# Optimization experiments

Measured on AMD Instinct MI355X. Metric: run time of the kernel, lower is better.

The kernel has to match this reference:

```python
import jax, jax.numpy as jnp
import numpy as np

N = 50000
E = 600000
IN, HID, OUT = 128, 128, 64
EPS = 1e-5

def setup_inputs() -> dict:
    key = jax.random.key(0)
    ks = jax.random.split(key, 16)
    def lin(k, i, o):
        s = 1.0 / np.sqrt(i)
        return jax.random.uniform(k, (i, o), jnp.float32, -s, s)
    inp = {
        "x": jax.random.normal(ks[0], (N, IN), jnp.float32),
        "edge_index": jax.random.randint(ks[1], (2, E), 0, N, jnp.int32),
        "edge_weight": jax.random.uniform(ks[2], (E,), jnp.float32),
        # SAGEConv params: lin_l (aggregated neighbors, with bias), lin_r (root)
        "Wl0": lin(ks[3], IN, HID), "Wr0": lin(ks[4], IN, HID), "b0": jnp.zeros((HID,), jnp.float32),
        "Wl1": lin(ks[5], HID, HID), "Wr1": lin(ks[6], HID, HID), "b1": jnp.zeros((HID,), jnp.float32),
        "Wl2": lin(ks[7], HID, OUT), "Wr2": lin(ks[8], HID, OUT), "b2": jnp.zeros((OUT,), jnp.float32),
        "gamma0": jnp.ones((HID,), jnp.float32), "beta0": jnp.zeros((HID,), jnp.float32),
        "gamma1": jnp.ones((HID,), jnp.float32), "beta1": jnp.zeros((HID,), jnp.float32),
    }
    return inp

def _sage_conv(x, src, dst, w, Wl, Wr, b):
    # weighted message m_e = w_e * x[src_e], mean-aggregated at dst
    msg = x[src] * w[:, None]                                   # [E, F]
    agg = jax.ops.segment_sum(msg, dst, num_segments=N)          # [N, F]
    cnt = jax.ops.segment_sum(jnp.ones_like(w), dst, num_segments=N)
    mean = agg / jnp.maximum(cnt, 1.0)[:, None]
    return mean @ Wl + b + x @ Wr

def _bn(x, gamma, beta):
    mu = jnp.mean(x, axis=0)
    var = jnp.var(x, axis=0)
    return (x - mu) * jax.lax.rsqrt(var + EPS) * gamma + beta

def reference(x, edge_index, edge_weight,
              Wl0, Wr0, b0, Wl1, Wr1, b1, Wl2, Wr2, b2,
              gamma0, beta0, gamma1, beta1):
    src, dst = edge_index[0], edge_index[1]
    h = _sage_conv(x, src, dst, edge_weight, Wl0, Wr0, b0)
    h = jax.nn.relu(_bn(h, gamma0, beta0))  # dropout: identity in eval
    h = _sage_conv(h, src, dst, edge_weight, Wl1, Wr1, b1)
    h = jax.nn.relu(_bn(h, gamma1, beta1))
    return _sage_conv(h, src, dst, edge_weight, Wl2, Wr2, b2)
```

## Files before the change

### kernel.cpp

```cpp
#include <hip/hip_runtime.h>
#include <hip/hip_bf16.h>

#define NN 50000
#define EE 600000
#define SREP 64
#define SCB 49

typedef short bf16x8 __attribute__((ext_vector_type(8)));
typedef float f32x4 __attribute__((ext_vector_type(4)));

__device__ inline ushort f2bf(float x) {
  unsigned u = __float_as_uint(x);
  u = (u + 0x7fffu + ((u >> 16) & 1u)) >> 16;
  return (ushort)u;
}
__device__ inline float bflo(uint t) { return __uint_as_float(t << 16); }
__device__ inline float bfhi(uint t) { return __uint_as_float(t & 0xffff0000u); }
__device__ inline uint f22bf(float a, float b) { return ((uint)f2bf(b) << 16) | (uint)f2bf(a); }

__global__ void count_k(const int* __restrict__ ei, int* __restrict__ cnt_d) {
  int e = blockIdx.x * 256 + threadIdx.x;
  if (e < EE) atomicAdd(&cnt_d[ei[EE + e]], 1);
}

__global__ __launch_bounds__(256) void scanA_k(const int* __restrict__ cnt,
                                               int* __restrict__ cur,
                                               int* __restrict__ bsum) {
  __shared__ int ls[256];
  const int t = threadIdx.x;
  const int base = blockIdx.x * 1024 + t * 4;
  int4 v = {0, 0, 0, 0};
  if (base + 3 < NN) v = *(const int4*)(cnt + base);
  else {
    if (base + 0 < NN) v.x = cnt[base + 0];
    if (base + 1 < NN) v.y = cnt[base + 1];
    if (base + 2 < NN) v.z = cnt[base + 2];
  }
  ls[t] = v.x + v.y + v.z + v.w;
  __syncthreads();
  for (int off = 1; off < 256; off <<= 1) {
    int u = (t >= off) ? ls[t - off] : 0;
    __syncthreads();
    ls[t] += u;
    __syncthreads();
  }
  int ex = (t == 0) ? 0 : ls[t - 1];
  int4 o;
  o.x = ex;
  o.y = ex + v.x;
  o.z = o.y + v.y;
  o.w = o.z + v.z;
  if (base + 3 < NN) *(int4*)(cur + base) = o;
  else {
    if (base + 0 < NN) cur[base + 0] = o.x;
    if (base + 1 < NN) cur[base + 1] = o.y;
    if (base + 2 < NN) cur[base + 2] = o.z;
  }
  if (t == 255) bsum[blockIdx.x] = ls[255];
}

__global__ __launch_bounds__(64) void scanB_k(int* __restrict__ bsum) {
  int t = threadIdx.x;
  int own = (t < SCB) ? bsum[t] : 0;
  int v = own;
#pragma unroll
  for (int off = 1; off < 64; off <<= 1) {
    int u = __shfl_up(v, off, 64);
    if (t >= off) v += u;
  }
  if (t < SCB) bsum[t] = v - own;
}

__global__ __launch_bounds__(256) void scanC_k(int* __restrict__ cur,
                                               const int* __restrict__ bsum,
                                               const int* __restrict__ cnt_d,
                                               int* __restrict__ rowp,
                                               float* __restrict__ invd) {
  const int t = threadIdx.x;
  const int base = blockIdx.x * 1024 + t * 4;
  const int off = bsum[blockIdx.x];
  if (base + 3 < NN) {
    int4 v = *(int4*)(cur + base);
    v.x += off; v.y += off; v.z += off; v.w += off;
    *(int4*)(cur + base) = v;
    *(int4*)(rowp + base) = v;
    int4 cd = *(const int4*)(cnt_d + base);
    float4 iv;
    iv.x = 1.0f / (float)max(cd.x, 1);
    iv.y = 1.0f / (float)max(cd.y, 1);
    iv.z = 1.0f / (float)max(cd.z, 1);
    iv.w = 1.0f / (float)max(cd.w, 1);
    *(float4*)(invd + base) = iv;
  } else {
    for (int i = 0; i < 4; ++i) {
      if (base + i < NN) {
        int v = cur[base + i] + off;
        cur[base + i] = v;
        rowp[base + i] = v;
        invd[base + i] = 1.0f / (float)max(cnt_d[base + i], 1);
      }
    }
  }
}

__global__ void fill_k(const int* __restrict__ ei, const float* __restrict__ ew,
                       int* __restrict__ cur_d, int2* __restrict__ eL) {
  int e = blockIdx.x * 256 + threadIdx.x;
  if (e < EE) {
    int s = ei[e], d = ei[EE + e];
    int pc = atomicAdd(&cur_d[d], 1);
    int2 v;
    v.x = s;
    v.y = __float_as_int(ew[e]);
    eL[pc] = v;
  }
}

__global__ void wpk_k(const float* __restrict__ Wl0, const float* __restrict__ Wr0,
                      const float* __restrict__ Wl1, const float* __restrict__ Wr1,
                      const float* __restrict__ Wl2, const float* __restrict__ Wr2,
                      ushort* __restrict__ wbuf) {
  int idx = blockIdx.x * 256 + threadIdx.x;
  const float* W; int F, r, off;
  if (idx < 16384)      { W = Wl0; F = 128; r = idx;         off = 0; }
  else if (idx < 32768) { W = Wr0; F = 128; r = idx - 16384; off = 16384; }
  else if (idx < 49152) { W = Wl1; F = 128; r = idx - 32768; off = 32768; }
  else if (idx < 65536) { W = Wr1; F = 128; r = idx - 49152; off = 49152; }
  else if (idx < 73728) { W = Wl2; F = 64;  r = idx - 65536; off = 65536; }
  else                  { W = Wr2; F = 64;  r = idx - 73728; off = 73728; }
  int k = r / F, n = r % F;
  wbuf[off + n * 128 + ((((k >> 3) + n) & 15) << 3) + (k & 7)] = f2bf(W[k * F + n]);
}

template <int F, bool HB16>
__global__ __launch_bounds__(256) void gemm_mfma(
    const void* __restrict__ H, const ushort* __restrict__ Wpre,
    const float* __restrict__ ss, ushort* __restrict__ Tlb,
    ushort* __restrict__ Trb) {
  __shared__ __align__(16) ushort Wt[F * 128];
  const int tid = threadIdx.x;
  const int lane = tid & 63;
  const int w = tid >> 6;
  const int col = lane & 15;
  const int quad = lane >> 4;
  const int nb = blockIdx.x * 128;

  bf16x8 afrag[2][4];
#pragma unroll
  for (int t2 = 0; t2 < 2; ++t2) {
    const int row = nb + w * 32 + t2 * 16 + col;
#pragma unroll
    for (int s = 0; s < 4; ++s) {
      const int c = s * 4 + quad;
      const int gk = c * 8;
      uint4 hv = {0, 0, 0, 0};
      if (HB16) {
        if (row < NN) hv = *(const uint4*)((const ushort*)H + (size_t)row * 128 + gk);
        uint* p = (uint*)&hv;
#pragma unroll
        for (int j = 0; j < 4; ++j) {
          float f0 = fmaxf(fmaf(bflo(p[j]), ss[gk + 2 * j], ss[128 + gk + 2 * j]), 0.f);
          float f1 = fmaxf(fmaf(bfhi(p[j]), ss[gk + 2 * j + 1], ss[128 + gk + 2 * j + 1]), 0.f);
          p[j] = f22bf(f0, f1);
        }
      } else {
        float4 fa = {0.f, 0.f, 0.f, 0.f}, fb = {0.f, 0.f, 0.f, 0.f};
        if (row < NN) {
          fa = *(const float4*)((const float*)H + (size_t)row * 128 + gk);
          fb = *(const float4*)((const float*)H + (size_t)row * 128 + gk + 4);
        }
        uint* p = (uint*)&hv;
        p[0] = f22bf(fa.x, fa.y);
        p[1] = f22bf(fa.z, fa.w);
        p[2] = f22bf(fb.x, fb.y);
        p[3] = f22bf(fb.z, fb.w);
      }
      afrag[t2][s] = *(const bf16x8*)&hv;
    }
  }

  for (int phase = 0; phase < 2; ++phase) {
    const uint4* src = (const uint4*)(Wpre + phase * F * 128);
    __syncthreads();
    for (int i = tid; i < F * 16; i += 256) ((uint4*)Wt)[i] = src[i];
    __syncthreads();
    ushort* Outp = phase ? Trb : Tlb;
#pragma unroll 2
    for (int ct = 0; ct < F / 16; ++ct) {
      const int n = ct * 16 + col;
      f32x4 acc0 = {0.f, 0.f, 0.f, 0.f};
      f32x4 acc1 = {0.f, 0.f, 0.f, 0.f};
#pragma unroll
      for (int s = 0; s < 4; ++s) {
        const int c = s * 4 + quad;
        bf16x8 b = *(const bf16x8*)&Wt[n * 128 + (((c + n) & 15) << 3)];
        acc0 = __builtin_amdgcn_mfma_f32_16x16x32_bf16(afrag[0][s], b, acc0, 0, 0, 0);
        acc1 = __builtin_amdgcn_mfma_f32_16x16x32_bf16(afrag[1][s], b, acc1, 0, 0, 0);
      }
      const int cc = ct * 16 + col;
      const int nodeb0 = nb + w * 32 + quad * 4;
#pragma unroll
      for (int r = 0; r < 4; ++r) {
        const int node = nodeb0 + r;
        if (node < NN) Outp[(size_t)node * F + cc] = f2bf(acc0[r]);
      }
#pragma unroll
      for (int r = 0; r < 4; ++r) {
        const int node = nodeb0 + 16 + r;
        if (node < NN) Outp[(size_t)node * F + cc] = f2bf(acc1[r]);
      }
    }
  }
}

template <int F, bool STATS, bool OUTF32>
__global__ __launch_bounds__(256, 8) void gather_combine(
    const ushort* __restrict__ Tlb, const int2* __restrict__ eL,
    const int* __restrict__ rowp, const int* __restrict__ cnt_d,
    const ushort* __restrict__ Trb, const float* __restrict__ invd,
    const float* __restrict__ bias, void* __restrict__ outp,
    float* __restrict__ statsb) {
  constexpr int L = F / 2;
  constexpr int NPI = 256 / L;
  constexpr int NPB = (L == 64) ? 20 : 16;
  const int tid = threadIdx.x;
  const int cp = tid % L;
  const int c = 2 * cp;
  const int nl = tid / L;
  const int n0 = blockIdx.x * NPB;
  const float bx = bias[c], by = bias[c + 1];
  float2 S = {0.f, 0.f}, Q = {0.f, 0.f};
#pragma unroll
  for (int it = 0; it < NPB / NPI; ++it) {
    int n = n0 + it * NPI + nl;
    if constexpr (L == 64) n = __builtin_amdgcn_readfirstlane(n);
    const int beg = rowp[n];
    const int deg = cnt_d[n];
    float a0 = 0.f, a1 = 0.f;
    for (int base = 0; base < deg; base += L) {
      const int take = deg - base;
      int2 er = {0, 0};
      if (cp < take) er = eL[beg + base + cp];
      int m = take < L ? take : L;
      if constexpr (L == 32) m = max(m, __shfl_xor(m, 32, 64));
      int j = 0;
      for (; j + 4 <= m; j += 4) {
        int s0 = __shfl(er.x, j + 0, L);
        int s1 = __shfl(er.x, j + 1, L);
        int s2 = __shfl(er.x, j + 2, L);
        int s3 = __shfl(er.x, j + 3, L);
        float w0 = __int_as_float(__shfl(er.y, j + 0, L));
        float w1 = __int_as_float(__shfl(er.y, j + 1, L));
        float w2 = __int_as_float(__shfl(er.y, j + 2, L));
        float w3 = __int_as_float(__shfl(er.y, j + 3, L));
        uint t0 = ((const uint*)Tlb)[(size_t)s0 * L + cp];
        uint t1 = ((const uint*)Tlb)[(size_t)s1 * L + cp];
        uint t2 = ((const uint*)Tlb)[(size_t)s2 * L + cp];
        uint t3 = ((const uint*)Tlb)[(size_t)s3 * L + cp];
        a0 = fmaf(w0, bflo(t0), a0); a1 = fmaf(w0, bfhi(t0), a1);
        a0 = fmaf(w1, bflo(t1), a0); a1 = fmaf(w1, bfhi(t1), a1);
        a0 = fmaf(w2, bflo(t2), a0); a1 = fmaf(w2, bfhi(t2), a1);
        a0 = fmaf(w3, bflo(t3), a0); a1 = fmaf(w3, bfhi(t3), a1);
      }
      for (; j < m; ++j) {
        int s0 = __shfl(er.x, j, L);
        float w0 = __int_as_float(__shfl(er.y, j, L));
        uint t0 = ((const uint*)Tlb)[(size_t)s0 * L + cp];
        a0 = fmaf(w0, bflo(t0), a0);
        a1 = fmaf(w0, bfhi(t0), a1);
      }
    }
    float iv = invd[n];
    uint tb = ((const uint*)Trb)[(size_t)n * L + cp];
    float2 v;
    v.x = fmaf(a0, iv, bflo(tb) + bx);
    v.y = fmaf(a1, iv, bfhi(tb) + by);
    if (OUTF32) *(float2*)((float*)outp + (size_t)n * F + c) = v;
    else ((uint*)outp)[(size_t)n * L + cp] = f22bf(v.x, v.y);
    if constexpr (STATS) {
      S.x += v.x; S.y += v.y;
      Q.x += v.x * v.x; Q.y += v.y * v.y;
    }
  }
  if constexpr (STATS) {
    __shared__ float2 sS[4][L];
    __shared__ float2 sQ[4][L];
    const int wid = tid >> 6, wl = tid & 63;
    if constexpr (L == 64) {
      sS[wid][wl] = S;
      sQ[wid][wl] = Q;
    } else {
      S.x += __shfl_xor(S.x, 32, 64); S.y += __shfl_xor(S.y, 32, 64);
      Q.x += __shfl_xor(Q.x, 32, 64); Q.y += __shfl_xor(Q.y, 32, 64);
      if (wl < 32) { sS[wid][wl] = S; sQ[wid][wl] = Q; }
    }
    __syncthreads();
    if (tid < L) {
      float2 Sa = sS[0][tid], Qa = sQ[0][tid];
#pragma unroll
      for (int w2 = 1; w2 < 4; ++w2) {
        Sa.x += sS[w2][tid].x; Sa.y += sS[w2][tid].y;
        Qa.x += sQ[w2][tid].x; Qa.y += sQ[w2][tid].y;
      }
      float* sb = statsb + (size_t)(blockIdx.x & (SREP - 1)) * 256;
      int col = 2 * tid;
      atomicAdd(&sb[col], Sa.x);
      atomicAdd(&sb[col + 1], Sa.y);
      atomicAdd(&sb[128 + col], Qa.x);
      atomicAdd(&sb[128 + col + 1], Qa.y);
    }
  }
}

__global__ void bn_fin(float* __restrict__ statsb, const float* __restrict__ gamma,
                       const float* __restrict__ beta, float* __restrict__ ss) {
  int f = threadIdx.x;
  float sum = 0.f, sq = 0.f;
#pragma unroll 8
  for (int r = 0; r < SREP; ++r) {
    sum += statsb[r * 256 + f];
    sq  += statsb[r * 256 + 128 + f];
    statsb[r * 256 + f] = 0.f;
    statsb[r * 256 + 128 + f] = 0.f;
  }
  float mu = sum * (1.0f / (float)NN);
  float ex2 = sq * (1.0f / (float)NN);
  float var = ex2 - mu * mu;
  float sc = gamma[f] * rsqrtf(var + 1e-5f);
  ss[f] = sc;
  ss[128 + f] = beta[f] - mu * sc;
}

extern "C" void kernel_launch(void* const* d_in, const int* in_sizes, int n_in,
                              void* d_out, int out_size, void* d_ws, size_t ws_size,
                              hipStream_t stream) {
  (void)in_sizes; (void)n_in; (void)out_size; (void)ws_size;
  const float* x   = (const float*)d_in[0];
  const int*   ei  = (const int*)d_in[1];
  const float* ew  = (const float*)d_in[2];
  const float* Wl0 = (const float*)d_in[3];
  const float* Wr0 = (const float*)d_in[4];
  const float* b0  = (const float*)d_in[5];
  const float* Wl1 = (const float*)d_in[6];
  const float* Wr1 = (const float*)d_in[7];
  const float* b1  = (const float*)d_in[8];
  const float* Wl2 = (const float*)d_in[9];
  const float* Wr2 = (const float*)d_in[10];
  const float* b2  = (const float*)d_in[11];
  const float* g0  = (const float*)d_in[12];
  const float* be0 = (const float*)d_in[13];
  const float* g1  = (const float*)d_in[14];
  const float* be1 = (const float*)d_in[15];
  float* out = (float*)d_out;

  size_t off = 0;
  auto alloc = [&](size_t b) -> void* {
    void* p = (char*)d_ws + off;
    off += (b + 255) & ~(size_t)255;
    return p;
  };
  ushort* tlb  = (ushort*)alloc((size_t)NN * 128 * 2);
  ushort* trb  = (ushort*)alloc((size_t)NN * 128 * 2);
  ushort* hpre = (ushort*)alloc((size_t)NN * 128 * 2);
  int2* eL     = (int2*)alloc((size_t)EE * 8);
  ushort* wbuf = (ushort*)alloc(81920 * 2);
  int*  cnt_d  = (int*)alloc((size_t)NN * 4);
  int*  cur_d  = (int*)alloc((size_t)NN * 4);
  int*  rowp   = (int*)alloc((size_t)NN * 4);
  int*  bsum   = (int*)alloc(SCB * 4);
  float* invd  = (float*)alloc((size_t)NN * 4);
  float* statsb = (float*)alloc((size_t)SREP * 256 * 4);
  float* ssb   = (float*)alloc(256 * 4);

  const int EB = (EE + 255) / 256;
  const int GEMMB = (NN + 127) / 128;

  hipMemsetAsync(cnt_d, 0, (size_t)NN * 4, stream);
  hipMemsetAsync(statsb, 0, (size_t)SREP * 256 * 4, stream);
  count_k<<<EB, 256, 0, stream>>>(ei, cnt_d);
  wpk_k<<<320, 256, 0, stream>>>(Wl0, Wr0, Wl1, Wr1, Wl2, Wr2, wbuf);
  scanA_k<<<SCB, 256, 0, stream>>>(cnt_d, cur_d, bsum);
  scanB_k<<<1, 64, 0, stream>>>(bsum);
  scanC_k<<<SCB, 256, 0, stream>>>(cur_d, bsum, cnt_d, rowp, invd);
  fill_k<<<EB, 256, 0, stream>>>(ei, ew, cur_d, eL);

  const int GB128 = NN / 20;
  const int GB64  = NN / 16;

  gemm_mfma<128, false><<<GEMMB, 256, 0, stream>>>(x, wbuf, nullptr, tlb, trb);
  gather_combine<128, true, false><<<GB128, 256, 0, stream>>>(tlb, eL, rowp, cnt_d, trb, invd, b0, hpre, statsb);
  bn_fin<<<1, 128, 0, stream>>>(statsb, g0, be0, ssb);

  gemm_mfma<128, true><<<GEMMB, 256, 0, stream>>>(hpre, wbuf + 32768, ssb, tlb, trb);
  gather_combine<128, true, false><<<GB128, 256, 0, stream>>>(tlb, eL, rowp, cnt_d, trb, invd, b1, hpre, statsb);
  bn_fin<<<1, 128, 0, stream>>>(statsb, g1, be1, ssb);

  gemm_mfma<64, true><<<GEMMB, 256, 0, stream>>>(hpre, wbuf + 65536, ssb, tlb, trb);
  gather_combine<64, false, true><<<GB64, 256, 0, stream>>>(tlb, eL, rowp, cnt_d, trb, invd, b2, out, nullptr);
}
```

Measured before the change: 312.4 us.

## Cut kernel launches by fusing prep kernels, scan pass, and BN finalize

New measurement: 303.2 us. -2.9%, faster.

```diff
diff --git a/kernel.cpp b/kernel.cpp
--- a/kernel.cpp
+++ b/kernel.cpp
@@ -18,9 +18,29 @@
 __device__ inline float bfhi(uint t) { return __uint_as_float(t & 0xffff0000u); }
 __device__ inline uint f22bf(float a, float b) { return ((uint)f2bf(b) << 16) | (uint)f2bf(a); }
 
-__global__ void count_k(const int* __restrict__ ei, int* __restrict__ cnt_d) {
-  int e = blockIdx.x * 256 + threadIdx.x;
-  if (e < EE) atomicAdd(&cnt_d[ei[EE + e]], 1);
+#define EB 2344
+
+__global__ void prep0_k(const int* __restrict__ ei, int* __restrict__ cnt_d,
+                        const float* __restrict__ Wl0, const float* __restrict__ Wr0,
+                        const float* __restrict__ Wl1, const float* __restrict__ Wr1,
+                        const float* __restrict__ Wl2, const float* __restrict__ Wr2,
+                        ushort* __restrict__ wbuf) {
+  const int b = blockIdx.x;
+  if (b < EB) {
+    int e = b * 256 + threadIdx.x;
+    if (e < EE) atomicAdd(&cnt_d[ei[EE + e]], 1);
+  } else {
+    int idx = (b - EB) * 256 + threadIdx.x;
+    const float* W; int F, r, off;
+    if (idx < 16384)      { W = Wl0; F = 128; r = idx;         off = 0; }
+    else if (idx < 32768) { W = Wr0; F = 128; r = idx - 16384; off = 16384; }
+    else if (idx < 49152) { W = Wl1; F = 128; r = idx - 32768; off = 32768; }
+    else if (idx < 65536) { W = Wr1; F = 128; r = idx - 49152; off = 49152; }
+    else if (idx < 73728) { W = Wl2; F = 64;  r = idx - 65536; off = 65536; }
+    else                  { W = Wr2; F = 64;  r = idx - 73728; off = 73728; }
+    int k = r / F, n = r % F;
+    wbuf[off + n * 128 + ((((k >> 3) + n) & 15) << 3) + (k & 7)] = f2bf(W[k * F + n]);
+  }
 }
 
 __global__ __launch_bounds__(256) void scanA_k(const int* __restrict__ cnt,
@@ -59,26 +79,28 @@
   if (t == 255) bsum[blockIdx.x] = ls[255];
 }
 
-__global__ __launch_bounds__(64) void scanB_k(int* __restrict__ bsum) {
-  int t = threadIdx.x;
-  int own = (t < SCB) ? bsum[t] : 0;
-  int v = own;
-#pragma unroll
-  for (int off = 1; off < 64; off <<= 1) {
-    int u = __shfl_up(v, off, 64);
-    if (t >= off) v += u;
-  }
-  if (t < SCB) bsum[t] = v - own;
-}
-
 __global__ __launch_bounds__(256) void scanC_k(int* __restrict__ cur,
                                                const int* __restrict__ bsum,
                                                const int* __restrict__ cnt_d,
                                                int* __restrict__ rowp,
                                                float* __restrict__ invd) {
+  __shared__ int soff;
   const int t = threadIdx.x;
+  if (t < 64) {
+    int own = (t < SCB) ? bsum[t] : 0;
+    int v = own;
+#pragma unroll
+    for (int o = 1; o < 64; o <<= 1) {
+      int u = __shfl_up(v, o, 64);
+      if (t >= o) v += u;
+    }
+    int incl = __shfl(v, blockIdx.x, 64);
+    int ownb = __shfl(own, blockIdx.x, 64);
+    if (t == 0) soff = incl - ownb;
+  }
+  __syncthreads();
+  const int off = soff;
   const int base = blockIdx.x * 1024 + t * 4;
-  const int off = bsum[blockIdx.x];
   if (base + 3 < NN) {
     int4 v = *(int4*)(cur + base);
     v.x += off; v.y += off; v.z += off; v.w += off;
@@ -116,34 +138,37 @@
   }
 }
 
-__global__ void wpk_k(const float* __restrict__ Wl0, const float* __restrict__ Wr0,
-                      const float* __restrict__ Wl1, const float* __restrict__ Wr1,
-                      const float* __restrict__ Wl2, const float* __restrict__ Wr2,
-                      ushort* __restrict__ wbuf) {
-  int idx = blockIdx.x * 256 + threadIdx.x;
-  const float* W; int F, r, off;
-  if (idx < 16384)      { W = Wl0; F = 128; r = idx;         off = 0; }
-  else if (idx < 32768) { W = Wr0; F = 128; r = idx - 16384; off = 16384; }
-  else if (idx < 49152) { W = Wl1; F = 128; r = idx - 32768; off = 32768; }
-  else if (idx < 65536) { W = Wr1; F = 128; r = idx - 49152; off = 49152; }
-  else if (idx < 73728) { W = Wl2; F = 64;  r = idx - 65536; off = 65536; }
-  else                  { W = Wr2; F = 64;  r = idx - 73728; off = 73728; }
-  int k = r / F, n = r % F;
-  wbuf[off + n * 128 + ((((k >> 3) + n) & 15) << 3) + (k & 7)] = f2bf(W[k * F + n]);
-}
-
 template <int F, bool HB16>
 __global__ __launch_bounds__(256) void gemm_mfma(
     const void* __restrict__ H, const ushort* __restrict__ Wpre,
-    const float* __restrict__ ss, ushort* __restrict__ Tlb,
+    const float* __restrict__ statsb, const float* __restrict__ gamma,
+    const float* __restrict__ beta, ushort* __restrict__ Tlb,
     ushort* __restrict__ Trb) {
   __shared__ __align__(16) ushort Wt[F * 128];
+  __shared__ float ssl[256];
   const int tid = threadIdx.x;
   const int lane = tid & 63;
   const int w = tid >> 6;
   const int col = lane & 15;
   const int quad = lane >> 4;
   const int nb = blockIdx.x * 128;
+
+  if (HB16) {
+    float s = 0.f;
+#pragma unroll 8
+    for (int r = 0; r < SREP; ++r) s += statsb[r * 256 + tid];
+    ssl[tid] = s;
+    __syncthreads();
+    if (tid < 128) {
+      float mu = ssl[tid] * (1.0f / (float)NN);
+      float ex2 = ssl[128 + tid] * (1.0f / (float)NN);
+      float var = ex2 - mu * mu;
+      float sc = gamma[tid] * rsqrtf(var + 1e-5f);
+      ssl[tid] = sc;
+      ssl[128 + tid] = beta[tid] - mu * sc;
+    }
+    __syncthreads();
+  }
 
   bf16x8 afrag[2][4];
 #pragma unroll
@@ -159,8 +184,8 @@
         uint* p = (uint*)&hv;
 #pragma unroll
         for (int j = 0; j < 4; ++j) {
-          float f0 = fmaxf(fmaf(bflo(p[j]), ss[gk + 2 * j], ss[128 + gk + 2 * j]), 0.f);
-          float f1 = fmaxf(fmaf(bfhi(p[j]), ss[gk + 2 * j + 1], ss[128 + gk + 2 * j + 1]), 0.f);
+          float f0 = fmaxf(fmaf(bflo(p[j]), ssl[gk + 2 * j], ssl[128 + gk + 2 * j]), 0.f);
+          float f1 = fmaxf(fmaf(bfhi(p[j]), ssl[gk + 2 * j + 1], ssl[128 + gk + 2 * j + 1]), 0.f);
           p[j] = f22bf(f0, f1);
         }
       } else {
@@ -312,25 +337,6 @@
   }
 }
 
-__global__ void bn_fin(float* __restrict__ statsb, const float* __restrict__ gamma,
-                       const float* __restrict__ beta, float* __restrict__ ss) {
-  int f = threadIdx.x;
-  float sum = 0.f, sq = 0.f;
-#pragma unroll 8
-  for (int r = 0; r < SREP; ++r) {
-    sum += statsb[r * 256 + f];
-    sq  += statsb[r * 256 + 128 + f];
-    statsb[r * 256 + f] = 0.f;
-    statsb[r * 256 + 128 + f] = 0.f;
-  }
-  float mu = sum * (1.0f / (float)NN);
-  float ex2 = sq * (1.0f / (float)NN);
-  float var = ex2 - mu * mu;
-  float sc = gamma[f] * rsqrtf(var + 1e-5f);
-  ss[f] = sc;
-  ss[128 + f] = beta[f] - mu * sc;
-}
-
 extern "C" void kernel_launch(void* const* d_in, const int* in_sizes, int n_in,
                               void* d_out, int out_size, void* d_ws, size_t ws_size,
                               hipStream_t stream) {
@@ -364,37 +370,33 @@
   ushort* hpre = (ushort*)alloc((size_t)NN * 128 * 2);
   int2* eL     = (int2*)alloc((size_t)EE * 8);
   ushort* wbuf = (ushort*)alloc(81920 * 2);
-  int*  cnt_d  = (int*)alloc((size_t)NN * 4);
+  const size_t CNT_B  = ((size_t)NN * 4 + 255) & ~(size_t)255;
+  const size_t STAT_B = (size_t)SREP * 256 * 4;
+  char* zb = (char*)alloc(CNT_B + 2 * STAT_B);
+  int*   cnt_d   = (int*)zb;
+  float* statsb0 = (float*)(zb + CNT_B);
+  float* statsb1 = (float*)(zb + CNT_B + STAT_B);
   int*  cur_d  = (int*)alloc((size_t)NN * 4);
   int*  rowp   = (int*)alloc((size_t)NN * 4);
   int*  bsum   = (int*)alloc(SCB * 4);
   float* invd  = (float*)alloc((size_t)NN * 4);
-  float* statsb = (float*)alloc((size_t)SREP * 256 * 4);
-  float* ssb   = (float*)alloc(256 * 4);
-
-  const int EB = (EE + 255) / 256;
+
   const int GEMMB = (NN + 127) / 128;
-
-  hipMemsetAsync(cnt_d, 0, (size_t)NN * 4, stream);
-  hipMemsetAsync(statsb, 0, (size_t)SREP * 256 * 4, stream);
-  count_k<<<EB, 256, 0, stream>>>(ei, cnt_d);
-  wpk_k<<<320, 256, 0, stream>>>(Wl0, Wr0, Wl1, Wr1, Wl2, Wr2, wbuf);
+  const int GB128 = NN / 20;
+  const int GB64  = NN / 16;
+
+  hipMemsetAsync(zb, 0, CNT_B + 2 * STAT_B, stream);
+  prep0_k<<<EB + 320, 256, 0, stream>>>(ei, cnt_d, Wl0, Wr0, Wl1, Wr1, Wl2, Wr2, wbuf);
   scanA_k<<<SCB, 256, 0, stream>>>(cnt_d, cur_d, bsum);
-  scanB_k<<<1, 64, 0, stream>>>(bsum);
   scanC_k<<<SCB, 256, 0, stream>>>(cur_d, bsum, cnt_d, rowp, invd);
   fill_k<<<EB, 256, 0, stream>>>(ei, ew, cur_d, eL);
 
-  const int GB128 = NN / 20;
-  const int GB64  = NN / 16;
-
-  gemm_mfma<128, false><<<GEMMB, 256, 0, stream>>>(x, wbuf, nullptr, tlb, trb);
-  gather_combine<128, true, false><<<GB128, 256, 0, stream>>>(tlb, eL, rowp, cnt_d, trb, invd, b0, hpre, statsb);
-  bn_fin<<<1, 128, 0, stream>>>(statsb, g0, be0, ssb);
-
-  gemm_mfma<128, true><<<GEMMB, 256, 0, stream>>>(hpre, wbuf + 32768, ssb, tlb, trb);
-  gather_combine<128, true, false><<<GB128, 256, 0, stream>>>(tlb, eL, rowp, cnt_d, trb, invd, b1, hpre, statsb);
-  bn_fin<<<1, 128, 0, stream>>>(statsb, g1, be1, ssb);
-
-  gemm_mfma<64, true><<<GEMMB, 256, 0, stream>>>(hpre, wbuf + 65536, ssb, tlb, trb);
+  gemm_mfma<128, false><<<GEMMB, 256, 0, stream>>>(x, wbuf, nullptr, nullptr, nullptr, tlb, trb);
+  gather_combine<128, true, false><<<GB128, 256, 0, stream>>>(tlb, eL, rowp, cnt_d, trb, invd, b0, hpre, statsb0);
+
+  gemm_mfma<128, true><<<GEMMB, 256, 0, stream>>>(hpre, wbuf + 32768, statsb0, g0, be0, tlb, trb);
+  gather_combine<128, true, false><<<GB128, 256, 0, stream>>>(tlb, eL, rowp, cnt_d, trb, invd, b1, hpre, statsb1);
+
+  gemm_mfma<64, true><<<GEMMB, 256, 0, stream>>>(hpre, wbuf + 65536, statsb1, g1, be1, tlb, trb);
   gather_combine<64, false, true><<<GB64, 256, 0, stream>>>(tlb, eL, rowp, cnt_d, trb, invd, b2, out, nullptr);
 }
```
